# Kernel tuning notes

Measured on AMD Instinct MI355X. Metric: run time of the kernel, lower is better.

Reference implementation:

```python
import jax, jax.numpy as jnp
import numpy as np

IH, IW = 32, 32
N = IH * IW            # tokens
C = 256                # inp == oup
HEADS, DH = 8, 32
INNER = HEADS * DH     # 256
HID = 2 * C            # 512
EPS = 1e-5
SCALE = DH ** -0.5


def _relative_index():
    ci = np.stack(np.meshgrid(np.arange(IH), np.arange(IW), indexing='ij')).reshape(2, -1)
    rel = ci[:, :, None] - ci[:, None, :]          # [2, n, n]
    rel[0] += IH - 1
    rel[1] += IW - 1
    rel[0] *= 2 * IW - 1
    return (rel[0] + rel[1]).astype(np.int32).reshape(-1)  # [n*n]


def setup_inputs() -> dict:
    key = jax.random.key(0)
    ks = jax.random.split(key, 12)
    B = 16
    s = lambda k, shape, scale=0.02: jax.random.normal(k, shape, jnp.float32) * scale
    return {
        'x': jax.random.normal(ks[0], (B, C, IH, IW), jnp.float32),
        'rel_index': jnp.asarray(_relative_index()),
        'ln1_g': jnp.ones((C,), jnp.float32),
        'ln1_b': jnp.zeros((C,), jnp.float32),
        'Wqkv': s(ks[1], (C, 3 * INNER)),
        'table': s(ks[2], ((2 * IH - 1) * (2 * IW - 1), HEADS)),
        'Wo': s(ks[3], (INNER, C)),
        'bo': jnp.zeros((C,), jnp.float32),
        'ln2_g': jnp.ones((C,), jnp.float32),
        'ln2_b': jnp.zeros((C,), jnp.float32),
        'W1': s(ks[4], (C, HID)),
        'b1': jnp.zeros((HID,), jnp.float32),
        'W2': s(ks[5], (HID, C)),
        'b2': jnp.zeros((C,), jnp.float32),
    }


def _ln(t, g, b):
    mu = t.mean(-1, keepdims=True)
    var = ((t - mu) ** 2).mean(-1, keepdims=True)
    return (t - mu) * jax.lax.rsqrt(var + EPS) * g + b


def reference(x, rel_index, ln1_g, ln1_b, Wqkv, table, Wo, bo, ln2_g, ln2_b, W1, b1, W2, b2):
    B = x.shape[0]
    t = jnp.transpose(x.reshape(B, C, N), (0, 2, 1))  # [B, n, C]
    # --- attention sub-block (PreNorm) ---
    h = _ln(t, ln1_g, ln1_b)
    qkv = h @ Wqkv                                    # [B, n, 3*inner]
    q, k, v = jnp.split(qkv, 3, axis=-1)
    tohd = lambda u: jnp.transpose(u.reshape(B, N, HEADS, DH), (0, 2, 1, 3))  # bhnd
    q, k, v = tohd(q), tohd(k), tohd(v)
    dots = jnp.einsum('bhnd,bhmd->bhnm', q, k) * SCALE
    bias = table[rel_index].reshape(N, N, HEADS).transpose(2, 0, 1)[None]  # [1,h,n,n]
    attn = jax.nn.softmax(dots + bias, axis=-1)
    out = jnp.einsum('bhnm,bhmd->bhnd', attn, v)
    out = jnp.transpose(out, (0, 2, 1, 3)).reshape(B, N, INNER)
    out = out @ Wo + bo
    t = t + out
    # --- feed-forward sub-block (PreNorm) ---
    h = _ln(t, ln2_g, ln2_b)
    h = jax.nn.gelu(h @ W1 + b1, approximate=False)
    h = h @ W2 + b2
    t = t + h
    return jnp.transpose(t, (0, 2, 1)).reshape(B, C, IH, IW)
```

## Files before the change

### kernel.cpp

```cpp
#include <hip/hip_runtime.h>
#include <hip/hip_bf16.h>
#include <math.h>

typedef __bf16 bfx4 __attribute__((ext_vector_type(4)));
typedef __bf16 bfx8 __attribute__((ext_vector_type(8)));
typedef float  f32x4 __attribute__((ext_vector_type(4)));

#define BATCH 16
#define NTOK  1024
#define CDIM  256
#define NHEAD 8
#define DHEAD 32
#define QKVD  768
#define INNER 256
#define SCALE 0.17677669529663687f
#define LOG2E 1.4426950408889634f

#if __has_builtin(__builtin_amdgcn_exp2f)
#define EXP2(x) __builtin_amdgcn_exp2f(x)
#else
#define EXP2(x) exp2f(x)
#endif

__launch_bounds__(256)
__global__ void txln_kernel(const float* __restrict__ x, const float* __restrict__ g,
                            const float* __restrict__ bb, __bf16* __restrict__ tb,
                            __bf16* __restrict__ hln) {
  __shared__ float tile[256][65];
  const int b = blockIdx.z, n0 = blockIdx.x * 64;
  const int tt = threadIdx.x;
  const float* src = x + (size_t)b * CDIM * NTOK;
  const int rc = tt >> 4, nc = (tt & 15) * 4;
  #pragma unroll
  for (int i = 0; i < 16; ++i) {
    int c = rc + i * 16;
    *(float4*)&tile[c][nc] = *(const float4*)&src[(size_t)c * NTOK + n0 + nc];
  }
  __syncthreads();
  const int n = tt >> 2, c0 = (tt & 3) * 64;
  float vals[64];
  float s = 0.f, s2 = 0.f;
  #pragma unroll
  for (int j = 0; j < 64; ++j) {
    float v = tile[c0 + j][n];
    vals[j] = v; s += v; s2 += v * v;
  }
  s  += __shfl_xor(s, 1);  s  += __shfl_xor(s, 2);
  s2 += __shfl_xor(s2, 1); s2 += __shfl_xor(s2, 2);
  float mu = s * 0.00390625f;
  float var = s2 * 0.00390625f - mu * mu;
  float rs = rsqrtf(var + 1e-5f);
  size_t row = ((size_t)b * NTOK + n0 + n) * CDIM;
  #pragma unroll
  for (int j = 0; j < 64; j += 4) {
    const float4 gg = *(const float4*)&g[c0 + j];
    const float4 bv = *(const float4*)&bb[c0 + j];
    bfx4 tv;
    tv[0] = (__bf16)vals[j];     tv[1] = (__bf16)vals[j + 1];
    tv[2] = (__bf16)vals[j + 2]; tv[3] = (__bf16)vals[j + 3];
    *(bfx4*)&tb[row + c0 + j] = tv;
    bfx4 o;
    o[0] = (__bf16)((vals[j]     - mu) * rs * gg.x + bv.x);
    o[1] = (__bf16)((vals[j + 1] - mu) * rs * gg.y + bv.y);
    o[2] = (__bf16)((vals[j + 2] - mu) * rs * gg.z + bv.z);
    o[3] = (__bf16)((vals[j + 3] - mu) * rs * gg.w + bv.w);
    *(bfx4*)&hln[row + c0 + j] = o;
  }
}

__launch_bounds__(256)
__global__ void ln_kernel(const __bf16* __restrict__ in, const float* __restrict__ g,
                          const float* __restrict__ bb, __bf16* __restrict__ out) {
  int row  = blockIdx.x * 4 + (threadIdx.x >> 6);
  int lane = threadIdx.x & 63;
  const bfx4 vb = *(const bfx4*)(in + (size_t)row * 256 + lane * 4);
  float4 v;
  v.x = (float)vb[0]; v.y = (float)vb[1]; v.z = (float)vb[2]; v.w = (float)vb[3];
  float s  = v.x + v.y + v.z + v.w;
  float s2 = v.x * v.x + v.y * v.y + v.z * v.z + v.w * v.w;
  #pragma unroll
  for (int o = 32; o; o >>= 1) { s += __shfl_xor(s, o); s2 += __shfl_xor(s2, o); }
  float mu  = s * 0.00390625f;
  float var = s2 * 0.00390625f - mu * mu;
  float rs  = rsqrtf(var + 1e-5f);
  const float4 gg = ((const float4*)g)[lane];
  const float4 bv = ((const float4*)bb)[lane];
  bfx4 o4;
  o4[0] = (__bf16)((v.x - mu) * rs * gg.x + bv.x);
  o4[1] = (__bf16)((v.y - mu) * rs * gg.y + bv.y);
  o4[2] = (__bf16)((v.z - mu) * rs * gg.z + bv.z);
  o4[3] = (__bf16)((v.w - mu) * rs * gg.w + bv.w);
  *(bfx4*)(out + (size_t)row * 256 + lane * 4) = o4;
}

__launch_bounds__(256)
__global__ void wprep4_kernel(const float* __restrict__ Wqkv, const float* __restrict__ Wo,
                              const float* __restrict__ W1, const float* __restrict__ W2,
                              __bf16* __restrict__ Wqkvt, __bf16* __restrict__ Wot,
                              __bf16* __restrict__ W1t, __bf16* __restrict__ W2t) {
  int idx = blockIdx.x * 256 + threadIdx.x;
  const float* W; __bf16* Wt; int lk, Nn, off;
  if (idx < 196608)      { W = Wqkv; Wt = Wqkvt; lk = 8; Nn = 768; off = idx; }
  else if (idx < 262144) { W = Wo;   Wt = Wot;   lk = 8; Nn = 256; off = idx - 196608; }
  else if (idx < 393216) { W = W1;   Wt = W1t;   lk = 8; Nn = 512; off = idx - 262144; }
  else                   { W = W2;   Wt = W2t;   lk = 9; Nn = 256; off = idx - 393216; }
  int n = off >> lk, k = off & ((1 << lk) - 1);
  Wt[off] = (__bf16)W[(size_t)k * Nn + n];
}

__launch_bounds__(256)
__global__ void bias_kernel(const float* __restrict__ table, __bf16* __restrict__ biasB) {
  int idx = blockIdx.x * 256 + threadIdx.x;
  int k8 = (idx & 127) * 8, q = (idx >> 7) & 1023, h = idx >> 17;
  int qi = q >> 5, qj = q & 31;
  bfx8 o;
  #pragma unroll
  for (int j = 0; j < 8; ++j) {
    int k = k8 + j, ki = k >> 5, kj = k & 31;
    int r = (qi - ki + 31) * 63 + (qj - kj + 31);
    o[j] = (__bf16)(table[r * 8 + h] * LOG2E);
  }
  *(bfx8*)&biasB[((size_t)idx) * 8] = o;
}

template <int EPI>
__launch_bounds__(256)
__global__ void gemm128_kernel(const __bf16* __restrict__ A, const __bf16* __restrict__ Bt,
                               const float* __restrict__ bias,
                               const __bf16* __restrict__ residb,
                               void* __restrict__ outp, __bf16* __restrict__ vTout,
                               int Nn, int K) {
  __shared__ char smem[36864];
  __bf16 (*As)[72] = (__bf16(*)[72])smem;
  __bf16 (*Bs)[72] = (__bf16(*)[72])(smem + 18432);
  const int t = threadIdx.x, lane = t & 63, w = t >> 6;
  const int m0 = blockIdx.x * 128, n0 = blockIdx.y * 128;
  const int wr = w >> 1, wc = w & 1;
  const int lr = lane & 15, kb = (lane >> 4) * 4;
  int srow[4], sp0[4], sp1[4];
  #pragma unroll
  for (int i = 0; i < 4; ++i) {
    int cid = i * 256 + t, kb8 = (cid & 7) * 8;
    srow[i] = cid >> 3;
    int b0 = kb8, b1 = kb8 + 4;
    sp0[i] = (b0 & 32) + ((b0 & 12) << 1) + (((b0 >> 4) & 1) << 2) + (b0 & 3);
    sp1[i] = (b1 & 32) + ((b1 & 12) << 1) + (((b1 >> 4) & 1) << 2) + (b1 & 3);
  }
  f32x4 acc[4][4] = {};
  bfx8 ra[4], rb[4];
  auto gload = [&](int k0) {
    #pragma unroll
    for (int i = 0; i < 4; ++i) {
      int kc8 = ((i * 256 + t) & 7) * 8;
      ra[i] = *(const bfx8*)&A[(size_t)(m0 + srow[i]) * K + k0 + kc8];
      rb[i] = *(const bfx8*)&Bt[(size_t)(n0 + srow[i]) * K + k0 + kc8];
    }
  };
  gload(0);
  for (int k0 = 0; k0 < K; k0 += 64) {
    __syncthreads();
    #pragma unroll
    for (int i = 0; i < 4; ++i) {
      *(bfx4*)&As[srow[i]][sp0[i]] = __builtin_shufflevector(ra[i], ra[i], 0, 1, 2, 3);
      *(bfx4*)&As[srow[i]][sp1[i]] = __builtin_shufflevector(ra[i], ra[i], 4, 5, 6, 7);
      *(bfx4*)&Bs[srow[i]][sp0[i]] = __builtin_shufflevector(rb[i], rb[i], 0, 1, 2, 3);
      *(bfx4*)&Bs[srow[i]][sp1[i]] = __builtin_shufflevector(rb[i], rb[i], 4, 5, 6, 7);
    }
    __syncthreads();
    if (k0 + 64 < K) gload(k0 + 64);
    #pragma unroll
    for (int ks = 0; ks < 2; ++ks) {
      bfx8 af[4], bf[4];
      #pragma unroll
      for (int mi = 0; mi < 4; ++mi)
        af[mi] = *(const bfx8*)&As[wr * 64 + mi * 16 + lr][ks * 32 + kb * 2];
      #pragma unroll
      for (int ni = 0; ni < 4; ++ni)
        bf[ni] = *(const bfx8*)&Bs[wc * 64 + ni * 16 + lr][ks * 32 + kb * 2];
      #pragma unroll
      for (int mi = 0; mi < 4; ++mi)
        #pragma unroll
        for (int ni = 0; ni < 4; ++ni)
          acc[mi][ni] = __builtin_amdgcn_mfma_f32_16x16x32_bf16(af[mi], bf[ni],
                                                                acc[mi][ni], 0, 0, 0);
    }
  }
  if (EPI == 4) {
    float* Ty = (float*)smem;
    const int bb_ = m0 >> 10, tok0 = m0 & 1023;
    float* obase = (float*)outp + (size_t)bb_ * CDIM * NTOK + tok0;
    #pragma unroll
    for (int h2 = 0; h2 < 2; ++h2) {
      __syncthreads();
      if (wc == h2) {
        #pragma unroll
        for (int ni = 0; ni < 4; ++ni) {
          int ch = ni * 16 + lr;
          float bn = bias[n0 + h2 * 64 + ch];
          #pragma unroll
          for (int mi = 0; mi < 4; ++mi) {
            int tk = wr * 64 + mi * 16 + kb;
            float4 v4;
            #pragma unroll
            for (int r = 0; r < 4; ++r)
              ((float*)&v4)[r] = acc[mi][ni][r] + bn +
                  (float)residb[(size_t)(m0 + tk + r) * Nn + n0 + h2 * 64 + ch];
            *(float4*)&Ty[ch * 132 + tk] = v4;
          }
        }
      }
      __syncthreads();
      int ch = t >> 2, sc = t & 3;
      #pragma unroll
      for (int j = 0; j < 8; ++j) {
        int c4 = sc + j * 4;
        *(float4*)&obase[(size_t)(n0 + h2 * 64 + ch) * NTOK + c4 * 4] =
            *(const float4*)&Ty[ch * 132 + c4 * 4];
      }
    }
    return;
  }
  if (EPI == 0 && vTout != nullptr && n0 >= 512) {
    #pragma unroll
    for (int mi = 0; mi < 4; ++mi)
      #pragma unroll
      for (int ni = 0; ni < 4; ++ni) {
        int n = n0 + wc * 64 + ni * 16 + lr;
        int cp = n - 512, hh = cp >> 5, dd = cp & 31;
        int m = m0 + wr * 64 + mi * 16 + kb;
        int bb_ = m >> 10, tok = m & 1023;
        bfx4 o;
        o[0] = (__bf16)acc[mi][ni][0]; o[1] = (__bf16)acc[mi][ni][1];
        o[2] = (__bf16)acc[mi][ni][2]; o[3] = (__bf16)acc[mi][ni][3];
        *(bfx4*)&vTout[(((size_t)bb_ * NHEAD + hh) * DHEAD + dd) * NTOK + tok] = o;
      }
    return;
  }
  #pragma unroll
  for (int mi = 0; mi < 4; ++mi)
    #pragma unroll
    for (int ni = 0; ni < 4; ++ni)
      #pragma unroll
      for (int r = 0; r < 4; ++r) {
        int m = m0 + wr * 64 + mi * 16 + kb + r;
        int n = n0 + wc * 64 + ni * 16 + lr;
        float v = acc[mi][ni][r];
        if (EPI == 0) {
          ((__bf16*)outp)[(size_t)m * Nn + n] = (__bf16)v;
        } else if (EPI == 1) {
          v += bias[n] + (float)residb[(size_t)m * Nn + n];
          ((__bf16*)outp)[(size_t)m * Nn + n] = (__bf16)v;
        } else if (EPI == 2) {
          v += bias[n];
          v = 0.5f * v * (1.0f + erff(v * 0.70710678118f));
          ((__bf16*)outp)[(size_t)m * Nn + n] = (__bf16)v;
        }
      }
}

__launch_bounds__(512)
__global__ void attn_kernel(const __bf16* __restrict__ qkv, const __bf16* __restrict__ vT,
                            const __bf16* __restrict__ biasB, __bf16* __restrict__ outb) {
  __shared__ __bf16 Ks[64][40];
  __shared__ __bf16 Vs[32][72];
  __shared__ __bf16 Bls[256][72];
  const int q0 = blockIdx.x * 256, h = blockIdx.y, b = blockIdx.z;
  const int t = threadIdx.x, lane = t & 63, w = t >> 6;
  const int lr = lane & 15, kb = (lane >> 4) * 4;
  const size_t qbase = (size_t)b * NTOK * QKVD;
  const float qsc = SCALE * LOG2E;
  bfx8 qf[2];
  #pragma unroll
  for (int tq = 0; tq < 2; ++tq) {
    const __bf16* qp = &qkv[qbase + (size_t)(q0 + 32 * w + 16 * tq + lr) * QKVD + h * DHEAD];
    bfx4 lo = *(const bfx4*)&qp[kb];
    bfx4 hi = *(const bfx4*)&qp[kb + 16];
    #pragma unroll
    for (int j = 0; j < 4; ++j) {
      qf[tq][j]     = (__bf16)((float)lo[j] * qsc);
      qf[tq][j + 4] = (__bf16)((float)hi[j] * qsc);
    }
  }
  float l_run[2] = {0.f, 0.f};
  f32x4 oacc[2][2] = {};
  const int st_ = t & 255;
  const int krow = st_ >> 2, kc8 = (st_ & 3) * 8;
  const int vrow = st_ >> 3, vc8 = (st_ & 7) * 8;
  const __bf16* kvptr = (t < 256)
      ? &qkv[qbase + (size_t)krow * QKVD + INNER + h * DHEAD + kc8]
      : &vT[(((size_t)b * NHEAD + h) * DHEAD + vrow) * NTOK + vc8];
  const __bf16* bbase = &biasB[((size_t)h * NTOK + q0) * NTOK];
  bfx8 rkv, rbias[4];
  auto issue = [&](int k0) {
    rkv = (t < 256) ? *(const bfx8*)&kvptr[(size_t)k0 * QKVD]
                    : *(const bfx8*)&kvptr[k0];
    #pragma unroll
    for (int j = 0; j < 4; ++j) {
      int lin = j * 512 + t;
      int br = lin >> 3, bc8 = (lin & 7) * 8;
      rbias[j] = *(const bfx8*)&bbase[(size_t)br * NTOK + k0 + bc8];
    }
  };
  issue(0);
  for (int kt = 0; kt < 16; ++kt) {
    __syncthreads();
    if (t < 256) *(bfx8*)&Ks[krow][kc8] = rkv;
    else         *(bfx8*)&Vs[vrow][vc8] = rkv;
    #pragma unroll
    for (int j = 0; j < 4; ++j) {
      int lin = j * 512 + t;
      int br = lin >> 3, bc8 = (lin & 7) * 8;
      *(bfx8*)&Bls[br][bc8] = rbias[j];
    }
    __syncthreads();
    if (kt < 15) issue((kt + 1) * 64);
    bfx8 kf[4], vfr[4];
    #pragma unroll
    for (int f = 0; f < 4; ++f) {
      bfx4 klo = *(const bfx4*)&Ks[16 * f + lr][kb];
      bfx4 khi = *(const bfx4*)&Ks[16 * f + lr][kb + 16];
      kf[f] = __builtin_shufflevector(klo, khi, 0, 1, 2, 3, 4, 5, 6, 7);
    }
    #pragma unroll
    for (int s = 0; s < 2; ++s)
      #pragma unroll
      for (int df = 0; df < 2; ++df) {
        bfx4 vlo = *(const bfx4*)&Vs[16 * df + lr][s * 32 + kb];
        bfx4 vhi = *(const bfx4*)&Vs[16 * df + lr][s * 32 + kb + 16];
        vfr[s * 2 + df] = __builtin_shufflevector(vlo, vhi, 0, 1, 2, 3, 4, 5, 6, 7);
      }
    #pragma unroll
    for (int tq = 0; tq < 2; ++tq) {
      const int qrow_l = 32 * w + 16 * tq + lr;
      f32x4 st[4];
      #pragma unroll
      for (int f = 0; f < 4; ++f) {
        bfx4 bv = *(const bfx4*)&Bls[qrow_l][16 * f + kb];
        f32x4 c;
        c[0] = (float)bv[0]; c[1] = (float)bv[1];
        c[2] = (float)bv[2]; c[3] = (float)bv[3];
        st[f] = __builtin_amdgcn_mfma_f32_16x16x32_bf16(kf[f], qf[tq], c, 0, 0, 0);
      }
      float p[4][4], tsum = 0.f;
      #pragma unroll
      for (int f = 0; f < 4; ++f)
        #pragma unroll
        for (int r = 0; r < 4; ++r) {
          float e = EXP2(st[f][r]);
          p[f][r] = e;
          tsum += e;
        }
      l_run[tq] += tsum;
      bfx8 pa0, pa1;
      #pragma unroll
      for (int r = 0; r < 4; ++r) {
        pa0[r] = (__bf16)p[0][r];  pa0[r + 4] = (__bf16)p[1][r];
        pa1[r] = (__bf16)p[2][r];  pa1[r + 4] = (__bf16)p[3][r];
      }
      #pragma unroll
      for (int s = 0; s < 2; ++s) {
        bfx8 pa = s ? pa1 : pa0;
        #pragma unroll
        for (int df = 0; df < 2; ++df)
          oacc[tq][df] = __builtin_amdgcn_mfma_f32_16x16x32_bf16(pa, vfr[s * 2 + df],
                                                                 oacc[tq][df], 0, 0, 0);
      }
    }
  }
  #pragma unroll
  for (int tq = 0; tq < 2; ++tq) {
    float l = l_run[tq];
    l += __shfl_xor(l, 16);
    l += __shfl_xor(l, 32);
    float il[4];
    #pragma unroll
    for (int r = 0; r < 4; ++r) il[r] = 1.f / __shfl(l, kb + r);
    #pragma unroll
    for (int r = 0; r < 4; ++r) {
      size_t rowoff = (size_t)b * NTOK * CDIM +
                      (size_t)(q0 + 32 * w + 16 * tq + kb + r) * CDIM + h * DHEAD;
      outb[rowoff + lr]      = (__bf16)(oacc[tq][0][r] * il[r]);
      outb[rowoff + 16 + lr] = (__bf16)(oacc[tq][1][r] * il[r]);
    }
  }
}

extern "C" void kernel_launch(void* const* d_in, const int* in_sizes, int n_in,
                              void* d_out, int out_size, void* d_ws, size_t ws_size,
                              hipStream_t stream) {
  const float* x     = (const float*)d_in[0];
  const float* ln1_g = (const float*)d_in[2];
  const float* ln1_b = (const float*)d_in[3];
  const float* Wqkv  = (const float*)d_in[4];
  const float* table = (const float*)d_in[5];
  const float* Wo    = (const float*)d_in[6];
  const float* bo    = (const float*)d_in[7];
  const float* ln2_g = (const float*)d_in[8];
  const float* ln2_b = (const float*)d_in[9];
  const float* W1    = (const float*)d_in[10];
  const float* b1    = (const float*)d_in[11];
  const float* W2    = (const float*)d_in[12];
  const float* b2    = (const float*)d_in[13];

  char* ws = (char*)d_ws;
  __bf16* t_bf  = (__bf16*)(ws + 0);
  __bf16* t2_bf = (__bf16*)(ws + 8388608);
  __bf16* qkv   = (__bf16*)(ws + 33554432);
  __bf16* hln   = (__bf16*)(ws + 58720256);
  __bf16* aout  = (__bf16*)(ws + 67108864);
  __bf16* hid   = (__bf16*)(ws + 75497472);
  __bf16* vT    = (__bf16*)(ws + 75497472);
  __bf16* biasB = (__bf16*)(ws + 92274688);
  __bf16* Wqkvt = (__bf16*)(ws + 109051904);
  __bf16* Wot   = (__bf16*)(ws + 109445120);
  __bf16* W1t   = (__bf16*)(ws + 109576192);
  __bf16* W2t   = (__bf16*)(ws + 109838336);
  if (ws_size < 110100480) return;

  wprep4_kernel<<<2048, 256, 0, stream>>>(Wqkv, Wo, W1, W2, Wqkvt, Wot, W1t, W2t);
  bias_kernel<<<4096, 256, 0, stream>>>(table, biasB);
  txln_kernel<<<dim3(16, 1, 16), 256, 0, stream>>>(x, ln1_g, ln1_b, t_bf, hln);
  gemm128_kernel<0><<<dim3(128, 6), 256, 0, stream>>>(hln, Wqkvt, nullptr, nullptr, qkv, vT, 768, 256);
  attn_kernel<<<dim3(4, 8, 16), 512, 0, stream>>>(qkv, vT, biasB, aout);
  gemm128_kernel<1><<<dim3(128, 2), 256, 0, stream>>>(aout, Wot, bo, t_bf, t2_bf, nullptr, 256, 256);
  ln_kernel<<<4096, 256, 0, stream>>>(t2_bf, ln2_g, ln2_b, hln);
  gemm128_kernel<2><<<dim3(128, 4), 256, 0, stream>>>(hln, W1t, b1, nullptr, hid, nullptr, 512, 256);
  gemm128_kernel<4><<<dim3(128, 2), 256, 0, stream>>>(hid, W2t, b2, t2_bf, d_out, nullptr, 256, 512);
}
```

Baseline: 133.9 us.

## Load GEMM tiles directly into LDS with XOR-swizzled layout

Replaces the register-staged global-to-LDS copy in the 128x128 GEMM with direct global_load_lds 16-byte transfers and an XOR swizzle on the 16-byte chunk index, and adapts fragment reads to the swizzled layout. This removes VGPR staging and the separate LDS store instructions, and should reduce bank conflicts without padding. It also drops the register prefetch of the next k-tile, so global load latency is no longer overlapped with MFMA work within a block. The fragment read is now split into two 8-byte LDS reads.

```diff
diff --git a/kernel.cpp b/kernel.cpp
--- a/kernel.cpp
+++ b/kernel.cpp
@@ -21,6 +21,12 @@
 #else
 #define EXP2(x) exp2f(x)
 #endif
+
+__device__ __forceinline__ void gload_lds16(const __bf16* g, __bf16* l) {
+  __builtin_amdgcn_global_load_lds(
+      (const __attribute__((address_space(1))) unsigned int*)g,
+      (__attribute__((address_space(3))) unsigned int*)l, 16, 0, 0);
+}
 
 __launch_bounds__(256)
 __global__ void txln_kernel(const float* __restrict__ x, const float* __restrict__ g,
@@ -123,6 +129,17 @@
   *(bfx8*)&biasB[((size_t)idx) * 8] = o;
 }
 
+__device__ __forceinline__ bfx8 frag_read(const __bf16* base, int row, int ks, int kb) {
+  int blo = (ks * 32 + kb) * 2;
+  int bhi = blo + 32;
+  int slo = (blo & 15) | (((((blo >> 4) ^ row) & 7)) << 4);
+  int shi = (bhi & 15) | (((((bhi >> 4) ^ row) & 7)) << 4);
+  const char* rp = (const char*)base + row * 128;
+  bfx4 lo = *(const bfx4*)(rp + slo);
+  bfx4 hi = *(const bfx4*)(rp + shi);
+  return __builtin_shufflevector(lo, hi, 0, 1, 2, 3, 4, 5, 6, 7);
+}
+
 template <int EPI>
 __launch_bounds__(256)
 __global__ void gemm128_kernel(const __bf16* __restrict__ A, const __bf16* __restrict__ Bt,
@@ -131,52 +148,33 @@
                                void* __restrict__ outp, __bf16* __restrict__ vTout,
                                int Nn, int K) {
   __shared__ char smem[36864];
-  __bf16 (*As)[72] = (__bf16(*)[72])smem;
-  __bf16 (*Bs)[72] = (__bf16(*)[72])(smem + 18432);
+  __bf16* As = (__bf16*)smem;
+  __bf16* Bs = (__bf16*)(smem + 16384);
   const int t = threadIdx.x, lane = t & 63, w = t >> 6;
   const int m0 = blockIdx.x * 128, n0 = blockIdx.y * 128;
   const int wr = w >> 1, wc = w & 1;
   const int lr = lane & 15, kb = (lane >> 4) * 4;
-  int srow[4], sp0[4], sp1[4];
-  #pragma unroll
-  for (int i = 0; i < 4; ++i) {
-    int cid = i * 256 + t, kb8 = (cid & 7) * 8;
-    srow[i] = cid >> 3;
-    int b0 = kb8, b1 = kb8 + 4;
-    sp0[i] = (b0 & 32) + ((b0 & 12) << 1) + (((b0 >> 4) & 1) << 2) + (b0 & 3);
-    sp1[i] = (b1 & 32) + ((b1 & 12) << 1) + (((b1 >> 4) & 1) << 2) + (b1 & 3);
-  }
   f32x4 acc[4][4] = {};
-  bfx8 ra[4], rb[4];
-  auto gload = [&](int k0) {
-    #pragma unroll
-    for (int i = 0; i < 4; ++i) {
-      int kc8 = ((i * 256 + t) & 7) * 8;
-      ra[i] = *(const bfx8*)&A[(size_t)(m0 + srow[i]) * K + k0 + kc8];
-      rb[i] = *(const bfx8*)&Bt[(size_t)(n0 + srow[i]) * K + k0 + kc8];
-    }
-  };
-  gload(0);
   for (int k0 = 0; k0 < K; k0 += 64) {
     __syncthreads();
     #pragma unroll
     for (int i = 0; i < 4; ++i) {
-      *(bfx4*)&As[srow[i]][sp0[i]] = __builtin_shufflevector(ra[i], ra[i], 0, 1, 2, 3);
-      *(bfx4*)&As[srow[i]][sp1[i]] = __builtin_shufflevector(ra[i], ra[i], 4, 5, 6, 7);
-      *(bfx4*)&Bs[srow[i]][sp0[i]] = __builtin_shufflevector(rb[i], rb[i], 0, 1, 2, 3);
-      *(bfx4*)&Bs[srow[i]][sp1[i]] = __builtin_shufflevector(rb[i], rb[i], 4, 5, 6, 7);
+      int lin = i * 256 + t;
+      int r = lin >> 3, chunk = lin & 7;
+      int gc = (chunk ^ (r & 7)) * 8;
+      gload_lds16(&A[(size_t)(m0 + r) * K + k0 + gc], As + lin * 8);
+      gload_lds16(&Bt[(size_t)(n0 + r) * K + k0 + gc], Bs + lin * 8);
     }
     __syncthreads();
-    if (k0 + 64 < K) gload(k0 + 64);
     #pragma unroll
     for (int ks = 0; ks < 2; ++ks) {
       bfx8 af[4], bf[4];
       #pragma unroll
       for (int mi = 0; mi < 4; ++mi)
-        af[mi] = *(const bfx8*)&As[wr * 64 + mi * 16 + lr][ks * 32 + kb * 2];
+        af[mi] = frag_read(As, wr * 64 + mi * 16 + lr, ks, kb);
       #pragma unroll
       for (int ni = 0; ni < 4; ++ni)
-        bf[ni] = *(const bfx8*)&Bs[wc * 64 + ni * 16 + lr][ks * 32 + kb * 2];
+        bf[ni] = frag_read(Bs, wc * 64 + ni * 16 + lr, ks, kb);
       #pragma unroll
       for (int mi = 0; mi < 4; ++mi)
         #pragma unroll
```

New measurement: 139.6 us. 4.2% more time.
